# Kernel optimization log

Measured on AMD Instinct MI355X. Metric: run time of the kernel, lower is better.

The kernel has to match this reference:

```python
import jax, jax.numpy as jnp
import numpy as np

HIDDEN = 1024
HEADS = 16
HEAD_DIM = HIDDEN // HEADS
SCALE = HEAD_DIM ** -0.5
NEG_INF = float(-2 ** 32 + 1)


def setup_inputs() -> dict:
    key = jax.random.key(0)
    ks = jax.random.split(key, 10)
    B, N = 8, 1024
    std = HIDDEN ** -0.5
    inp = {
        "query": jax.random.normal(ks[0], (B, N, HIDDEN), dtype=jnp.float32),
        "mask": jax.random.randint(ks[1], (B, N), 0, 2, dtype=jnp.int32),
        "Wq": jax.random.normal(ks[2], (HIDDEN, HIDDEN), dtype=jnp.float32) * std,
        "bq": jnp.zeros((HIDDEN,), dtype=jnp.float32),
        "Wk": jax.random.normal(ks[3], (HIDDEN, HIDDEN), dtype=jnp.float32) * std,
        "bk": jnp.zeros((HIDDEN,), dtype=jnp.float32),
        "Wv": jax.random.normal(ks[4], (HIDDEN, HIDDEN), dtype=jnp.float32) * std,
        "bv": jnp.zeros((HIDDEN,), dtype=jnp.float32),
        "Wo": jax.random.normal(ks[5], (HIDDEN, HIDDEN), dtype=jnp.float32) * std,
        "bo": jnp.zeros((HIDDEN,), dtype=jnp.float32),
    }
    return inp


def reference(query, mask, Wq, bq, Wk, bk, Wv, bv, Wo, bo):
    B, N, C = query.shape
    H, D = HEADS, HEAD_DIM
    # projections: [B,N,C] -> [B,H,N,D]
    q = (query @ Wq + bq).reshape(B, N, H, D).transpose(0, 2, 1, 3)
    k = (query @ Wk + bk).reshape(B, N, H, D).transpose(0, 2, 1, 3)
    v = (query @ Wv + bv).reshape(B, N, H, D).transpose(0, 2, 1, 3)
    # scores [B,H,N,S]
    attn = jnp.einsum("bhnd,bhsd->bhns", q, k) * SCALE
    # padding mask broadcast over query positions: mask [B,S] -> [B,1,1,S]
    m = mask[:, None, None, :]
    attn = jnp.where(m == 0, jnp.float32(NEG_INF), attn)
    attn = jax.nn.softmax(attn, axis=-1)
    out = jnp.einsum("bhns,bhsd->bhnd", attn, v)
    out = out.transpose(0, 2, 1, 3).reshape(B, N, C)
    out = out @ Wo + bo
    return out
```

## Files before the change

### kernel.cpp

```cpp
#include <hip/hip_runtime.h>
#include <hip/hip_bf16.h>

typedef __bf16 bf16x8 __attribute__((ext_vector_type(8)));
typedef float f32x4 __attribute__((ext_vector_type(4)));
typedef float f32x16 __attribute__((ext_vector_type(16)));
typedef int i32x2 __attribute__((ext_vector_type(2)));
typedef __hip_bfloat16 bf16;

#define QK_SCALE 0.1803368801111204f

__device__ __forceinline__ f32x4 mfma_bf16(bf16x8 a, bf16x8 b, f32x4 c) {
  return __builtin_amdgcn_mfma_f32_16x16x32_bf16(a, b, c, 0, 0, 0);
}
__device__ __forceinline__ f32x16 mfma32(bf16x8 a, bf16x8 b, f32x16 c) {
  return __builtin_amdgcn_mfma_f32_32x32x16_bf16(a, b, c, 0, 0, 0);
}

__device__ __forceinline__ void gload16(const void* g, void* l) {
  __builtin_amdgcn_global_load_lds(
      (const __attribute__((address_space(1))) void*)g,
      (__attribute__((address_space(3))) void*)l, 16, 0, 0);
}

__global__ void cvt_bf16_kernel(const float* __restrict__ in, bf16* __restrict__ out) {
  int i = (blockIdx.x * 256 + threadIdx.x) * 4;
  float4 v = *reinterpret_cast<const float4*>(in + i);
  union { bf16 h[4]; uint2 u; } t;
  t.h[0] = __float2bfloat16(v.x);
  t.h[1] = __float2bfloat16(v.y);
  t.h[2] = __float2bfloat16(v.z);
  t.h[3] = __float2bfloat16(v.w);
  *reinterpret_cast<uint2*>(out + i) = t.u;
}

__global__ void transpose_w_kernel(const float* __restrict__ Wq, const float* __restrict__ Wk,
                                   const float* __restrict__ Wv, const float* __restrict__ Wo,
                                   bf16* __restrict__ Wqkv_t, bf16* __restrict__ Wot) {
  __shared__ float tile[32][33];
  int z = blockIdx.z;
  const float* src = (z == 0) ? Wq : (z == 1) ? Wk : (z == 2) ? Wv : Wo;
  bf16* dst = (z < 3) ? (Wqkv_t + (size_t)z * 1048576) : Wot;
  int tx = threadIdx.x, ty = threadIdx.y;
  int c0 = blockIdx.x * 32, r0 = blockIdx.y * 32;
#pragma unroll
  for (int i = 0; i < 32; i += 8)
    tile[ty + i][tx] = src[(r0 + ty + i) * 1024 + c0 + tx];
  __syncthreads();
#pragma unroll
  for (int i = 0; i < 32; i += 8)
    dst[(c0 + ty + i) * 1024 + r0 + tx] = __float2bfloat16(tile[tx][ty + i]);
}

__global__ __launch_bounds__(256) void gemm_qkv_kernel(
    const bf16* __restrict__ A, const bf16* __restrict__ Bt,
    const float* __restrict__ bq, const float* __restrict__ bk, const float* __restrict__ bv,
    bf16* __restrict__ Qb, bf16* __restrict__ Kb, bf16* __restrict__ Vt) {
  __shared__ __align__(16) bf16 As[2][128 * 32];
  __shared__ __align__(16) bf16 Bs[2][128 * 32];
  const int K = 1024;
  const int TILES_N = 24;
  const int NWG = 1536, CPX = NWG / 8;
  int bid0 = blockIdx.x;
  int bid = (bid0 % 8) * CPX + bid0 / 8;
  int bm = bid / TILES_N, bn = bid % TILES_N;
  int t = threadIdx.x;
  int lane = t & 63, w = t >> 6;
  int fr = lane & 15, fk = (lane >> 4) * 8;
  int wr = w >> 1, wc = w & 1;
  int srow = t >> 2, scol = (t & 3) * 8;

  const bf16* Ablk = A + (size_t)(bm * 128) * K;
  const bf16* Bblk = Bt + (size_t)(bn * 128) * K;

  auto stage = [&](int bufi, int k0) {
    char* ad = (char*)As[bufi] + t * 16;
    char* bd = (char*)Bs[bufi] + t * 16;
    gload16(Ablk + (size_t)srow * K + k0 + scol, ad);
    gload16(Ablk + (size_t)(srow + 64) * K + k0 + scol, ad + 4096);
    gload16(Bblk + (size_t)srow * K + k0 + scol, bd);
    gload16(Bblk + (size_t)(srow + 64) * K + k0 + scol, bd + 4096);
  };

  f32x4 acc[4][4] = {};

  stage(0, 0);
  __syncthreads();

  for (int k0 = 0; k0 < K; k0 += 32) {
    int cur = (k0 >> 5) & 1;
    if (k0 + 32 < K) stage(cur ^ 1, k0 + 32);
    bf16x8 a[4], b[4];
#pragma unroll
    for (int m = 0; m < 4; m++) a[m] = *(const bf16x8*)&As[cur][(wr * 64 + m * 16 + fr) * 32 + fk];
#pragma unroll
    for (int n = 0; n < 4; n++) b[n] = *(const bf16x8*)&Bs[cur][(wc * 64 + n * 16 + fr) * 32 + fk];
#pragma unroll
    for (int m = 0; m < 4; m++)
#pragma unroll
      for (int n = 0; n < 4; n++)
        acc[m][n] = mfma_bf16(a[m], b[n], acc[m][n]);
    __syncthreads();
  }

  int sel = (bn * 128) >> 10;
  const float* bias = (sel == 0) ? bq : (sel == 1) ? bk : bv;
#pragma unroll
  for (int m = 0; m < 4; m++) {
#pragma unroll
    for (int n = 0; n < 4; n++) {
      f32x4 c = acc[m][n];
      if (sel == 2) {
        int grow0 = bm * 128 + wr * 64 + m * 16 + (lane >> 4) * 4;
        int gcol = bn * 128 + wc * 64 + n * 16 + fr;
        int cc = gcol & 1023;
        int bb = grow0 >> 10, nr0 = grow0 & 1023;
        int h = cc >> 6, d = cc & 63;
        union { bf16 h4[4]; uint2 u; } o;
#pragma unroll
        for (int j = 0; j < 4; j++) o.h4[j] = __float2bfloat16(c[j] + bias[cc]);
        *(uint2*)&Vt[((size_t)(bb * 16 + h) * 64 + d) * 1024 + nr0] = o.u;
      } else {
#pragma unroll
        for (int j = 0; j < 4; j++) {
          int grow = bm * 128 + wr * 64 + m * 16 + (lane >> 4) * 4 + j;
          int gcol = bn * 128 + wc * 64 + n * 16 + fr;
          int cc = gcol & 1023;
          float val = c[j] + bias[cc];
          int bb = grow >> 10, nr = grow & 1023;
          int h = cc >> 6, d = cc & 63;
          int bh = bb * 16 + h;
          if (sel == 0) {
            Qb[((size_t)bh * 1024 + nr) * 64 + d] = __float2bfloat16(val * QK_SCALE);
          } else {
            Kb[((size_t)bh * 1024 + nr) * 64 + d] = __float2bfloat16(val);
          }
        }
      }
    }
  }
}

__global__ __launch_bounds__(256) void attn_kernel(
    const bf16* __restrict__ Qb, const bf16* __restrict__ Kb, const bf16* __restrict__ Vt,
    const int* __restrict__ mask, bf16* __restrict__ AO) {
  __shared__ unsigned pmw[32][2][8];
  __shared__ __align__(16) bf16 Ks[2][8192];
  __shared__ __align__(16) bf16 Vs[2][8192];

  int bid = blockIdx.x;
  int logical = (bid & 7) * 128 + (bid >> 3);
  int bh = logical >> 3;
  int qt = logical & 7;
  int b = bh >> 4, h = bh & 15;
  int t = threadIdx.x, w = t >> 6, lane = t & 63;
  int ql = lane & 31, hi = lane >> 5, hi8 = hi * 8;

#pragma unroll
  for (int rep = 0; rep < 2; rep++) {
    int idx = t + rep * 256;
    int T = idx >> 4, hh = (idx >> 3) & 1, i = idx & 7;
    int k0 = T * 32 + hh * 4 + 2 * (i & 1) + 8 * (i >> 1);
    unsigned lo = mask[b * 1024 + k0] ? 0xFFFFu : 0u;
    unsigned hg = mask[b * 1024 + k0 + 1] ? 0xFFFF0000u : 0u;
    pmw[T][hh][i] = lo | hg;
  }

  const bf16* Qh = Qb + (size_t)bh * 65536;
  const bf16* Kh = Kb + (size_t)bh * 65536;
  const bf16* Vh = Vt + (size_t)bh * 65536;

  int r0 = t >> 3;
  int sck = (t & 7) ^ (r0 & 7);
  int vd_row = r0 >> 1;
  int vpc = (r0 & 1) * 8 + (t & 7);

  auto stage = [&](int bufi, int kt) {
    char* kd = (char*)Ks[bufi] + t * 16;
    char* vd = (char*)Vs[bufi] + t * 16;
#pragma unroll
    for (int g = 0; g < 4; g++) {
      int kr = g * 32 + r0;
      gload16(Kh + (size_t)(kt + kr) * 64 + sck * 8, kd + g * 4096);
      int dvr = g * 16 + vd_row;
      int scv = vpc ^ (dvr & 15);
      gload16(Vh + (size_t)dvr * 1024 + kt + scv * 8, vd + g * 4096);
    }
  };

  int qn = qt * 128 + w * 32;
  bf16x8 qf[4];
#pragma unroll
  for (int c = 0; c < 4; c++)
    qf[c] = *(const bf16x8*)&Qh[(qn + ql) * 64 + c * 16 + hi8];

  bf16x8 ones;
#pragma unroll
  for (int j = 0; j < 8; j++) ones[j] = (__bf16)1.0f;

  f32x16 accO0 = {}, accO1 = {}, accL = {};

  stage(0, 0);
  __syncthreads();

  for (int kt = 0; kt < 1024; kt += 128) {
    int cur = (kt >> 7) & 1;
    if (kt + 128 < 1024) stage(cur ^ 1, kt + 128);
    const char* Kc = (const char*)Ks[cur];
    const char* Vc = (const char*)Vs[cur];

#pragma unroll
    for (int sub = 0; sub < 4; sub++) {
      int Ti = (kt >> 5) + sub;

      int krow = sub * 32 + ql;
      int ksw = (krow & 7) << 4;
      f32x16 s = {};
#pragma unroll
      for (int c = 0; c < 4; c++) {
        bf16x8 kf = *(const bf16x8*)(Kc + krow * 128 + ((c * 32 + hi * 16) ^ ksw));
        s = mfma32(kf, qf[c], s);
      }

#pragma unroll
      for (int r = 0; r < 16; r++) s[r] = __builtin_amdgcn_exp2f(s[r]);

      uint4 mwa = *(const uint4*)&pmw[Ti][hi][0];
      uint4 mwb = *(const uint4*)&pmw[Ti][hi][4];
      unsigned wds[8];
#pragma unroll
      for (int i = 0; i < 8; i++) {
        union { bf16 q[2]; unsigned u; } pk_;
        pk_.q[0] = __float2bfloat16(s[2 * i]);
        pk_.q[1] = __float2bfloat16(s[2 * i + 1]);
        wds[i] = pk_.u;
      }
      wds[0] &= mwa.x; wds[1] &= mwa.y; wds[2] &= mwa.z; wds[3] &= mwa.w;
      wds[4] &= mwb.x; wds[5] &= mwb.y; wds[6] &= mwb.z; wds[7] &= mwb.w;

      i32x2 r02 = __builtin_amdgcn_permlane32_swap((int)wds[0], (int)wds[2], false, false);
      i32x2 r13 = __builtin_amdgcn_permlane32_swap((int)wds[1], (int)wds[3], false, false);
      i32x2 r46 = __builtin_amdgcn_permlane32_swap((int)wds[4], (int)wds[6], false, false);
      i32x2 r57 = __builtin_amdgcn_permlane32_swap((int)wds[5], (int)wds[7], false, false);
      union { int i[4]; bf16x8 v; } y0, y1;
      y0.i[0] = r02[0]; y0.i[1] = r13[0]; y0.i[2] = r02[1]; y0.i[3] = r13[1];
      y1.i[0] = r46[0]; y1.i[1] = r57[0]; y1.i[2] = r46[1]; y1.i[3] = r57[1];

      int vr0 = ql, vr1 = 32 + ql;
      int x0 = vr0 & 15, x1 = vr1 & 15;
      int lcA = sub * 4 + hi, lcB = sub * 4 + 2 + hi;
      bf16x8 vc0 = *(const bf16x8*)(Vc + vr0 * 256 + ((lcA ^ x0) << 4));
      bf16x8 vc1 = *(const bf16x8*)(Vc + vr0 * 256 + ((lcB ^ x0) << 4));
      bf16x8 vc2 = *(const bf16x8*)(Vc + vr1 * 256 + ((lcA ^ x1) << 4));
      bf16x8 vc3 = *(const bf16x8*)(Vc + vr1 * 256 + ((lcB ^ x1) << 4));
      accO0 = mfma32(vc0, y0.v, accO0);
      accO0 = mfma32(vc1, y1.v, accO0);
      accO1 = mfma32(vc2, y0.v, accO1);
      accO1 = mfma32(vc3, y1.v, accO1);
      accL = mfma32(ones, y0.v, accL);
      accL = mfma32(ones, y1.v, accL);
    }
    __syncthreads();
  }

  float rl = 1.0f / accL[0];
  size_t rowbase = ((size_t)(b * 1024 + qn + ql)) * 1024 + h * 64;
#pragma unroll
  for (int dt = 0; dt < 2; dt++) {
#pragma unroll
    for (int q = 0; q < 4; q++) {
      union { bf16 h4[4]; uint2 u; } o;
#pragma unroll
      for (int j = 0; j < 4; j++) {
        float a = (dt == 0) ? accO0[4 * q + j] : accO1[4 * q + j];
        o.h4[j] = __float2bfloat16(a * rl);
      }
      *(uint2*)&AO[rowbase + dt * 32 + q * 8 + 4 * hi] = o.u;
    }
  }
}

__global__ __launch_bounds__(256) void gemm_out_kernel(
    const bf16* __restrict__ A, const bf16* __restrict__ Bt,
    const float* __restrict__ bo, float* __restrict__ Out) {
  __shared__ __align__(16) bf16 As[2][128 * 32];
  __shared__ __align__(16) bf16 Bs[2][128 * 32];
  const int K = 1024;
  const int TILES_N = 8;
  const int NWG = 512, CPX = NWG / 8;
  int bid0 = blockIdx.x;
  int bid = (bid0 % 8) * CPX + bid0 / 8;
  int bm = bid / TILES_N, bn = bid % TILES_N;
  int t = threadIdx.x;
  int lane = t & 63, w = t >> 6;
  int fr = lane & 15, fk = (lane >> 4) * 8;
  int wr = w >> 1, wc = w & 1;
  int srow = t >> 2, scol = (t & 3) * 8;

  const bf16* Ablk = A + (size_t)(bm * 128) * K;
  const bf16* Bblk = Bt + (size_t)(bn * 128) * K;

  auto stage = [&](int bufi, int k0) {
    char* ad = (char*)As[bufi] + t * 16;
    char* bd = (char*)Bs[bufi] + t * 16;
    gload16(Ablk + (size_t)srow * K + k0 + scol, ad);
    gload16(Ablk + (size_t)(srow + 64) * K + k0 + scol, ad + 4096);
    gload16(Bblk + (size_t)srow * K + k0 + scol, bd);
    gload16(Bblk + (size_t)(srow + 64) * K + k0 + scol, bd + 4096);
  };

  f32x4 acc[4][4] = {};

  stage(0, 0);
  __syncthreads();

  for (int k0 = 0; k0 < K; k0 += 32) {
    int cur = (k0 >> 5) & 1;
    if (k0 + 32 < K) stage(cur ^ 1, k0 + 32);
    bf16x8 a[4], b[4];
#pragma unroll
    for (int m = 0; m < 4; m++) a[m] = *(const bf16x8*)&As[cur][(wr * 64 + m * 16 + fr) * 32 + fk];
#pragma unroll
    for (int n = 0; n < 4; n++) b[n] = *(const bf16x8*)&Bs[cur][(wc * 64 + n * 16 + fr) * 32 + fk];
#pragma unroll
    for (int m = 0; m < 4; m++)
#pragma unroll
      for (int n = 0; n < 4; n++)
        acc[m][n] = mfma_bf16(a[m], b[n], acc[m][n]);
    __syncthreads();
  }

#pragma unroll
  for (int m = 0; m < 4; m++) {
#pragma unroll
    for (int n = 0; n < 4; n++) {
      f32x4 c = acc[m][n];
#pragma unroll
      for (int j = 0; j < 4; j++) {
        int grow = bm * 128 + wr * 64 + m * 16 + (lane >> 4) * 4 + j;
        int gcol = bn * 128 + wc * 64 + n * 16 + fr;
        Out[(size_t)grow * 1024 + gcol] = c[j] + bo[gcol];
      }
    }
  }
}

extern "C" void kernel_launch(void* const* d_in, const int* in_sizes, int n_in,
                              void* d_out, int out_size, void* d_ws, size_t ws_size,
                              hipStream_t stream) {
  const float* X = (const float*)d_in[0];
  const int* mask = (const int*)d_in[1];
  const float* Wq = (const float*)d_in[2];
  const float* bq = (const float*)d_in[3];
  const float* Wk = (const float*)d_in[4];
  const float* bk = (const float*)d_in[5];
  const float* Wv = (const float*)d_in[6];
  const float* bv = (const float*)d_in[7];
  const float* Wo = (const float*)d_in[8];
  const float* bo = (const float*)d_in[9];
  float* Out = (float*)d_out;

  char* ws = (char*)d_ws;
  bf16* Xb     = (bf16*)(ws + 0);
  bf16* Wqkv_t = (bf16*)(ws + 16777216);
  bf16* Wot    = (bf16*)(ws + 23068672);
  bf16* Qb     = (bf16*)(ws + 25165824);
  bf16* Kb     = (bf16*)(ws + 41943040);
  bf16* Vt     = (bf16*)(ws + 58720256);
  bf16* AO     = Xb;

  cvt_bf16_kernel<<<8192, 256, 0, stream>>>(X, Xb);
  transpose_w_kernel<<<dim3(32, 32, 4), dim3(32, 8), 0, stream>>>(Wq, Wk, Wv, Wo, Wqkv_t, Wot);
  gemm_qkv_kernel<<<1536, 256, 0, stream>>>(Xb, Wqkv_t, bq, bk, bv, Qb, Kb, Vt);
  attn_kernel<<<1024, 256, 0, stream>>>(Qb, Kb, Vt, mask, AO);
  gemm_out_kernel<<<512, 256, 0, stream>>>(AO, Wot, bo, Out);
}
```

Before: 157.8 us.

## Double GEMM K-tile to 64 with XOR-swizzled LDS layout in projections

Both the QKV and output projection GEMMs now stage 64-wide K slices instead of 32, which halves the number of loop iterations and barriers and doubles the MFMA work between syncs. The LDS tile rows are 128 bytes with a 16-byte chunk XOR swizzle keyed on the row, applied on the global-to-LDS store side and matched on the fragment reads, to avoid bank conflicts. LDS use per block doubles to 64 KB, which may cut how many blocks fit on a CU.

```diff
diff --git a/kernel.cpp b/kernel.cpp
--- a/kernel.cpp
+++ b/kernel.cpp
@@ -55,8 +55,8 @@
     const bf16* __restrict__ A, const bf16* __restrict__ Bt,
     const float* __restrict__ bq, const float* __restrict__ bk, const float* __restrict__ bv,
     bf16* __restrict__ Qb, bf16* __restrict__ Kb, bf16* __restrict__ Vt) {
-  __shared__ __align__(16) bf16 As[2][128 * 32];
-  __shared__ __align__(16) bf16 Bs[2][128 * 32];
+  __shared__ __align__(16) bf16 As[2][128 * 64];
+  __shared__ __align__(16) bf16 Bs[2][128 * 64];
   const int K = 1024;
   const int TILES_N = 24;
   const int NWG = 1536, CPX = NWG / 8;
@@ -65,9 +65,10 @@
   int bm = bid / TILES_N, bn = bid % TILES_N;
   int t = threadIdx.x;
   int lane = t & 63, w = t >> 6;
-  int fr = lane & 15, fk = (lane >> 4) * 8;
+  int fr = lane & 15, g4 = lane >> 4;
   int wr = w >> 1, wc = w & 1;
-  int srow = t >> 2, scol = (t & 3) * 8;
+  int srow8 = t >> 3;
+  int sc8 = (t & 7) ^ (srow8 & 7);
 
   const bf16* Ablk = A + (size_t)(bm * 128) * K;
   const bf16* Bblk = Bt + (size_t)(bn * 128) * K;
@@ -75,10 +76,11 @@
   auto stage = [&](int bufi, int k0) {
     char* ad = (char*)As[bufi] + t * 16;
     char* bd = (char*)Bs[bufi] + t * 16;
-    gload16(Ablk + (size_t)srow * K + k0 + scol, ad);
-    gload16(Ablk + (size_t)(srow + 64) * K + k0 + scol, ad + 4096);
-    gload16(Bblk + (size_t)srow * K + k0 + scol, bd);
-    gload16(Bblk + (size_t)(srow + 64) * K + k0 + scol, bd + 4096);
+#pragma unroll
+    for (int g = 0; g < 4; g++) {
+      gload16(Ablk + (size_t)(g * 32 + srow8) * K + k0 + sc8 * 8, ad + g * 4096);
+      gload16(Bblk + (size_t)(g * 32 + srow8) * K + k0 + sc8 * 8, bd + g * 4096);
+    }
   };
 
   f32x4 acc[4][4] = {};
@@ -86,19 +88,33 @@
   stage(0, 0);
   __syncthreads();
 
-  for (int k0 = 0; k0 < K; k0 += 32) {
-    int cur = (k0 >> 5) & 1;
-    if (k0 + 32 < K) stage(cur ^ 1, k0 + 32);
-    bf16x8 a[4], b[4];
-#pragma unroll
-    for (int m = 0; m < 4; m++) a[m] = *(const bf16x8*)&As[cur][(wr * 64 + m * 16 + fr) * 32 + fk];
-#pragma unroll
-    for (int n = 0; n < 4; n++) b[n] = *(const bf16x8*)&Bs[cur][(wc * 64 + n * 16 + fr) * 32 + fk];
+  for (int k0 = 0; k0 < K; k0 += 64) {
+    int cur = (k0 >> 6) & 1;
+    if (k0 + 64 < K) stage(cur ^ 1, k0 + 64);
+    const char* Ac = (const char*)As[cur];
+    const char* Bc = (const char*)Bs[cur];
+    bf16x8 a0[4], a1[4], b0[4], b1[4];
+#pragma unroll
+    for (int m = 0; m < 4; m++) {
+      int R = wr * 64 + m * 16 + fr;
+      int x = R & 7;
+      a0[m] = *(const bf16x8*)(Ac + R * 128 + ((g4 ^ x) << 4));
+      a1[m] = *(const bf16x8*)(Ac + R * 128 + (((4 + g4) ^ x) << 4));
+    }
+#pragma unroll
+    for (int n = 0; n < 4; n++) {
+      int R = wc * 64 + n * 16 + fr;
+      int x = R & 7;
+      b0[n] = *(const bf16x8*)(Bc + R * 128 + ((g4 ^ x) << 4));
+      b1[n] = *(const bf16x8*)(Bc + R * 128 + (((4 + g4) ^ x) << 4));
+    }
 #pragma unroll
     for (int m = 0; m < 4; m++)
 #pragma unroll
-      for (int n = 0; n < 4; n++)
-        acc[m][n] = mfma_bf16(a[m], b[n], acc[m][n]);
+      for (int n = 0; n < 4; n++) {
+        acc[m][n] = mfma_bf16(a0[m], b0[n], acc[m][n]);
+        acc[m][n] = mfma_bf16(a1[m], b1[n], acc[m][n]);
+      }
     __syncthreads();
   }
 
@@ -110,7 +126,7 @@
     for (int n = 0; n < 4; n++) {
       f32x4 c = acc[m][n];
       if (sel == 2) {
-        int grow0 = bm * 128 + wr * 64 + m * 16 + (lane >> 4) * 4;
+        int grow0 = bm * 128 + wr * 64 + m * 16 + g4 * 4;
         int gcol = bn * 128 + wc * 64 + n * 16 + fr;
         int cc = gcol & 1023;
         int bb = grow0 >> 10, nr0 = grow0 & 1023;
@@ -122,7 +138,7 @@
       } else {
 #pragma unroll
         for (int j = 0; j < 4; j++) {
-          int grow = bm * 128 + wr * 64 + m * 16 + (lane >> 4) * 4 + j;
+          int grow = bm * 128 + wr * 64 + m * 16 + g4 * 4 + j;
           int gcol = bn * 128 + wc * 64 + n * 16 + fr;
           int cc = gcol & 1023;
           float val = c[j] + bias[cc];
@@ -282,8 +298,8 @@
 __global__ __launch_bounds__(256) void gemm_out_kernel(
     const bf16* __restrict__ A, const bf16* __restrict__ Bt,
     const float* __restrict__ bo, float* __restrict__ Out) {
-  __shared__ __align__(16) bf16 As[2][128 * 32];
-  __shared__ __align__(16) bf16 Bs[2][128 * 32];
+  __shared__ __align__(16) bf16 As[2][128 * 64];
+  __shared__ __align__(16) bf16 Bs[2][128 * 64];
   const int K = 1024;
   const int TILES_N = 8;
   const int NWG = 512, CPX = NWG / 8;
@@ -292,9 +308,10 @@
   int bm = bid / TILES_N, bn = bid % TILES_N;
   int t = threadIdx.x;
   int lane = t & 63, w = t >> 6;
-  int fr = lane & 15, fk = (lane >> 4) * 8;
+  int fr = lane & 15, g4 = lane >> 4;
   int wr = w >> 1, wc = w & 1;
-  int srow = t >> 2, scol = (t & 3) * 8;
+  int srow8 = t >> 3;
+  int sc8 = (t & 7) ^ (srow8 & 7);
 
   const bf16* Ablk = A + (size_t)(bm * 128) * K;
   const bf16* Bblk = Bt + (size_t)(bn * 128) * K;
@@ -302,10 +319,11 @@
   auto stage = [&](int bufi, int k0) {
     char* ad = (char*)As[bufi] + t * 16;
     char* bd = (char*)Bs[bufi] + t * 16;
-    gload16(Ablk + (size_t)srow * K + k0 + scol, ad);
-    gload16(Ablk + (size_t)(srow + 64) * K + k0 + scol, ad + 4096);
-    gload16(Bblk + (size_t)srow * K + k0 + scol, bd);
-    gload16(Bblk + (size_t)(srow + 64) * K + k0 + scol, bd + 4096);
+#pragma unroll
+    for (int g = 0; g < 4; g++) {
+      gload16(Ablk + (size_t)(g * 32 + srow8) * K + k0 + sc8 * 8, ad + g * 4096);
+      gload16(Bblk + (size_t)(g * 32 + srow8) * K + k0 + sc8 * 8, bd + g * 4096);
+    }
   };
 
   f32x4 acc[4][4] = {};
@@ -313,19 +331,33 @@
   stage(0, 0);
   __syncthreads();
 
-  for (int k0 = 0; k0 < K; k0 += 32) {
-    int cur = (k0 >> 5) & 1;
-    if (k0 + 32 < K) stage(cur ^ 1, k0 + 32);
-    bf16x8 a[4], b[4];
-#pragma unroll
-    for (int m = 0; m < 4; m++) a[m] = *(const bf16x8*)&As[cur][(wr * 64 + m * 16 + fr) * 32 + fk];
-#pragma unroll
-    for (int n = 0; n < 4; n++) b[n] = *(const bf16x8*)&Bs[cur][(wc * 64 + n * 16 + fr) * 32 + fk];
+  for (int k0 = 0; k0 < K; k0 += 64) {
+    int cur = (k0 >> 6) & 1;
+    if (k0 + 64 < K) stage(cur ^ 1, k0 + 64);
+    const char* Ac = (const char*)As[cur];
+    const char* Bc = (const char*)Bs[cur];
+    bf16x8 a0[4], a1[4], b0[4], b1[4];
+#pragma unroll
+    for (int m = 0; m < 4; m++) {
+      int R = wr * 64 + m * 16 + fr;
+      int x = R & 7;
+      a0[m] = *(const bf16x8*)(Ac + R * 128 + ((g4 ^ x) << 4));
+      a1[m] = *(const bf16x8*)(Ac + R * 128 + (((4 + g4) ^ x) << 4));
+    }
+#pragma unroll
+    for (int n = 0; n < 4; n++) {
+      int R = wc * 64 + n * 16 + fr;
+      int x = R & 7;
+      b0[n] = *(const bf16x8*)(Bc + R * 128 + ((g4 ^ x) << 4));
+      b1[n] = *(const bf16x8*)(Bc + R * 128 + (((4 + g4) ^ x) << 4));
+    }
 #pragma unroll
     for (int m = 0; m < 4; m++)
 #pragma unroll
-      for (int n = 0; n < 4; n++)
-        acc[m][n] = mfma_bf16(a[m], b[n], acc[m][n]);
+      for (int n = 0; n < 4; n++) {
+        acc[m][n] = mfma_bf16(a0[m], b0[n], acc[m][n]);
+        acc[m][n] = mfma_bf16(a1[m], b1[n], acc[m][n]);
+      }
     __syncthreads();
   }
 
@@ -336,7 +368,7 @@
       f32x4 c = acc[m][n];
 #pragma unroll
       for (int j = 0; j < 4; j++) {
-        int grow = bm * 128 + wr * 64 + m * 16 + (lane >> 4) * 4 + j;
+        int grow = bm * 128 + wr * 64 + m * 16 + g4 * 4 + j;
         int gcol = bn * 128 + wc * 64 + n * 16 + fr;
         Out[(size_t)grow * 1024 + gcol] = c[j] + bo[gcol];
       }
```

After: 146.7 us, median of 2. 7.1% less time.
